# Kernel tuning notes

Hardware: AMD Instinct MI355X
Metric: run time of the kernel (lower is better)

## Reference

```python
import jax, jax.numpy as jnp
import numpy as np

D_MODEL = 1024
D_SAE = 16384
BATCH = 4096
EPS = 1e-8

def _layer_norm(v):
    # v: [B, D]; matches torch branch with keepdim=True
    mean = v.mean(axis=1, keepdims=True)
    var = ((v - mean) ** 2).mean(axis=1, keepdims=True)
    return (v - mean) / jnp.sqrt(var + EPS)

def setup_inputs() -> dict:
    key = jax.random.key(0)
    k1, k2 = jax.random.split(key)
    x = jax.random.normal(k1, (BATCH, 2 * D_MODEL), dtype=jnp.float32)
    # kaiming_uniform on [d_model, d_sae]: bound = sqrt(6 / fan_in), fan_in = d_sae (torch default mode='fan_in' on dim 1)
    bound = float(np.sqrt(6.0 / D_SAE))
    W_enc = jax.random.uniform(k2, (D_MODEL, D_SAE), dtype=jnp.float32, minval=-bound, maxval=bound)
    W_dec = W_enc.T  # init ties decoder to encoder transpose
    b_enc = jnp.zeros((D_SAE,), dtype=jnp.float32)
    b_dec = jnp.zeros((D_MODEL,), dtype=jnp.float32)
    return {"x": x, "W_enc": W_enc, "b_enc": b_enc, "W_dec": W_dec, "b_dec": b_dec, "k": 64}

def reference(x, W_enc, b_enc, W_dec, b_dec, k):
    B = x.shape[0]
    d_model = W_enc.shape[0]
    src = x[:, :d_model]
    tgt = x[:, d_model:]
    # standardize_method == 'layer_norm_and_diff_layer_norm'
    diff = _layer_norm(_layer_norm(tgt) - _layer_norm(src))  # [B, D]
    # encode
    acts = jax.nn.relu(diff @ W_enc + b_enc)  # [B, F]
    # batch top-k on decoder-norm-scaled scores
    dec_norms = jnp.linalg.norm(W_dec, axis=1)  # [F]
    flat_scores = (acts * dec_norms).reshape(-1)  # [B*F]
    _, topk_idx = jax.lax.top_k(flat_scores, k * B)
    mask = jnp.zeros_like(flat_scores).at[topk_idx].set(1.0).reshape(B, -1)
    sparse_acts = acts * mask  # [B, F]
    # decode
    recon = sparse_acts @ W_dec + b_dec  # [B, D]
    return recon
```

## Files before the change

kernel.cpp:

```cpp
#include <hip/hip_runtime.h>
#include <math.h>

#define D_MODEL 1024
#define D_SAE   16384
#define BATCH   4096
#define NTOT    (1ull * BATCH * D_SAE)
#define LN_EPS  1e-8
#define EPS_M   3e-4f
#define ROW_CAP 256
#define CAND_CAP  (4 * 1024 * 1024)
#define CAND2_CAP 65536

using bf16x8 = __attribute__((ext_vector_type(8))) short;
using f32x4  = __attribute__((ext_vector_type(4))) float;

__device__ inline unsigned short f2bf(float f) {
  unsigned u = __float_as_uint(f);
  return (unsigned short)((u + 0x7fffu + ((u >> 16) & 1u)) >> 16);
}
__device__ inline float bf2f(unsigned short h) {
  return __uint_as_float((unsigned)h << 16);
}

__device__ inline double blockReduceSum256(double v, double* lds) {
#pragma unroll
  for (int off = 32; off > 0; off >>= 1) v += __shfl_down(v, off, 64);
  int lane = threadIdx.x & 63, wid = threadIdx.x >> 6;
  __syncthreads();
  if (lane == 0) lds[wid] = v;
  __syncthreads();
  return lds[0] + lds[1] + lds[2] + lds[3];
}
__device__ inline int blockReduceSumInt256(int v, int* lds) {
#pragma unroll
  for (int off = 32; off > 0; off >>= 1) v += __shfl_down(v, off, 64);
  int lane = threadIdx.x & 63, wid = threadIdx.x >> 6;
  __syncthreads();
  if (lane == 0) lds[wid] = v;
  __syncthreads();
  return lds[0] + lds[1] + lds[2] + lds[3];
}

__device__ inline int wave_append(bool pred, int* counter) {
  unsigned long long m = __ballot(pred);
  int lane = threadIdx.x & 63;
  int pos = -1;
  if (m) {
    int ldr = __ffsll((long long)m) - 1;
    int base = 0;
    if (lane == ldr) base = atomicAdd(counter, __popcll(m));
    base = __shfl(base, ldr, 64);
    if (pred) pos = base + __popcll(m & ((1ull << lane) - 1ull));
  }
  return pos;
}

__device__ inline void hist_scan_desc(const int* __restrict__ hist, int nbins, int need,
                                      int& bsel, int& cumsel) {
  int t = threadIdx.x;
  int chunk = nbins >> 6;
  int topbase = nbins - t * chunk;
  int psum = 0;
  for (int i = 1; i <= chunk; ++i) psum += hist[topbase - i];
  int incl = psum;
#pragma unroll
  for (int off = 1; off < 64; off <<= 1) {
    int v = __shfl_up(incl, off, 64);
    if (t >= off) incl += v;
  }
  int excl = incl - psum;
  bool hit = (excl < need) && (excl + psum >= need);
  unsigned long long m = __ballot(hit);
  int tb = m ? (__ffsll((long long)m) - 1) : 63;
  int exb = __shfl(excl, tb, 64);
  int res_b = 0, res_c = 0;
  if (t == tb) {
    int c = exb;
    int b = nbins - tb * chunk - 1;
    int bend = b - chunk;
    for (; b > 0 && b > bend; --b) {
      int cc = hist[b];
      if (c + cc >= need) break;
      c += cc;
    }
    res_b = b; res_c = c;
  }
  bsel = __shfl(res_b, tb, 64);
  cumsel = __shfl(res_c, tb, 64);
}

__device__ inline void ln_row_fp64(const float* __restrict__ row, double* lds, double d[4]) {
  int t = threadIdx.x;
  float4 s4 = *(const float4*)(row + t * 4);
  float4 t4 = *(const float4*)(row + D_MODEL + t * 4);
  double s[4] = {s4.x, s4.y, s4.z, s4.w};
  double tt[4] = {t4.x, t4.y, t4.z, t4.w};
  double ms = blockReduceSum256(s[0] + s[1] + s[2] + s[3], lds) / D_MODEL;
  double mt = blockReduceSum256(tt[0] + tt[1] + tt[2] + tt[3], lds) / D_MODEL;
  double vs = 0, vt = 0;
#pragma unroll
  for (int i = 0; i < 4; i++) { double a = s[i] - ms; vs += a * a; a = tt[i] - mt; vt += a * a; }
  vs = blockReduceSum256(vs, lds) / D_MODEL;
  vt = blockReduceSum256(vt, lds) / D_MODEL;
  double rs = sqrt(vs + LN_EPS), rt = sqrt(vt + LN_EPS);
  double u[4];
#pragma unroll
  for (int i = 0; i < 4; i++) u[i] = (tt[i] - mt) / rt - (s[i] - ms) / rs;
  double mu = blockReduceSum256(u[0] + u[1] + u[2] + u[3], lds) / D_MODEL;
  double vu = 0;
#pragma unroll
  for (int i = 0; i < 4; i++) { double a = u[i] - mu; vu += a * a; }
  vu = blockReduceSum256(vu, lds) / D_MODEL;
  double ru = sqrt(vu + LN_EPS);
#pragma unroll
  for (int i = 0; i < 4; i++) d[i] = (u[i] - mu) / ru;
}

__global__ __launch_bounds__(256) void ln_kernel(const float* __restrict__ x,
                                                 short* __restrict__ Ahi, short* __restrict__ Alo) {
  __shared__ double lds[4];
  int b = blockIdx.x, t = threadIdx.x;
  double d[4];
  ln_row_fp64(x + (size_t)b * (2 * D_MODEL), lds, d);
  int mt = b >> 7, ml = b & 127;
  int ks = t >> 3, kc = (t >> 1) & 3, e0 = (t & 1) * 4;
  size_t base = ((((size_t)mt * 32 + ks) * 4 + kc) * 128 + ml) * 8 + e0;
  short h[4], l[4];
#pragma unroll
  for (int i = 0; i < 4; i++) {
    float f = (float)d[i];
    unsigned short hh = f2bf(f);
    h[i] = (short)hh;
    l[i] = (short)f2bf(f - bf2f(hh));
  }
  *(short4*)&Ahi[base] = make_short4(h[0], h[1], h[2], h[3]);
  *(short4*)&Alo[base] = make_short4(l[0], l[1], l[2], l[3]);
}

__global__ __launch_bounds__(256) void norm_kernel(const float* __restrict__ Wdec,
                                                   double* __restrict__ g64, float* __restrict__ g32) {
  __shared__ double lds[4];
  int j = blockIdx.x, t = threadIdx.x;
  float4 w = *(const float4*)(Wdec + (size_t)j * D_MODEL + t * 4);
  double a = (double)w.x * w.x + (double)w.y * w.y + (double)w.z * w.z + (double)w.w * w.w;
  double sum = blockReduceSum256(a, lds);
  if (t == 0) { double g = sqrt(sum); g64[j] = g; g32[j] = (float)g; }
}

__global__ __launch_bounds__(256) void wsplit_kernel(const float* __restrict__ Wenc,
                                                     short* __restrict__ Whi, short* __restrict__ Wlo) {
  __shared__ short sh[4096];
  __shared__ short sl[4096];
  int blk = blockIdx.x;
  int nt = blk >> 5, ks = blk & 31;
  int t = threadIdx.x;
  int r = t >> 3;
  int cg = t & 7;
  int kc = r >> 3, e = r & 7;
  const float* src = Wenc + (size_t)(ks * 32 + r) * D_SAE + nt * 128 + cg;
#pragma unroll
  for (int j = 0; j < 16; ++j) {
    float f = src[j * 8];
    unsigned short hh = f2bf(f);
    short ll = (short)f2bf(f - bf2f(hh));
    int c = j * 8 + cg;
    sh[kc * 1024 + c * 8 + e] = (short)hh;
    sl[kc * 1024 + c * 8 + e] = ll;
  }
  __syncthreads();
  size_t obase = ((size_t)nt * 32 + ks) * 4096;
  *(float4*)&Whi[obase + t * 16]     = *(const float4*)&sh[t * 16];
  *(float4*)&Whi[obase + t * 16 + 8] = *(const float4*)&sh[t * 16 + 8];
  *(float4*)&Wlo[obase + t * 16]     = *(const float4*)&sl[t * 16];
  *(float4*)&Wlo[obase + t * 16 + 8] = *(const float4*)&sl[t * 16 + 8];
}

__global__ __launch_bounds__(256) void hist_gemm(
    const short* __restrict__ Whi, const short* __restrict__ Ahi,
    const float* __restrict__ benc, const float* __restrict__ g32,
    int* __restrict__ ghist) {
  __shared__ short sA[4096];
  __shared__ short sB[4096];
  __shared__ int h[4][2048];
  const int tid = threadIdx.x;
  const int lane = tid & 63;
  const int w = tid >> 6;
  const int wm = (w >> 1) * 64, wn = (w & 1) * 64;
  int lin = blockIdx.x;
  int mt = lin >> 7, nt = lin & 127;
  const int col0 = nt * 128;
  for (int i = tid; i < 8192; i += 256) ((int*)h)[i] = 0;
  const size_t atile = (size_t)mt * 131072;
  const size_t btile = (size_t)nt * 131072;
  f32x4 acc[4][4] = {};
  const int kcl = lane >> 4, l15 = lane & 15;

  float4 a0, a1, b0, b1;
  {
    const float4* ah4 = (const float4*)(Ahi + atile);
    const float4* bh4 = (const float4*)(Whi + btile);
    a0 = ah4[tid]; a1 = ah4[tid + 256];
    b0 = bh4[tid]; b1 = bh4[tid + 256];
  }
  for (int ks = 0; ks < 32; ++ks) {
    __syncthreads();
    *(float4*)&sA[(size_t)tid * 8] = a0;
    *(float4*)&sA[(size_t)(tid + 256) * 8] = a1;
    *(float4*)&sB[(size_t)tid * 8] = b0;
    *(float4*)&sB[(size_t)(tid + 256) * 8] = b1;
    __syncthreads();
    if (ks < 31) {
      const float4* ah4 = (const float4*)(Ahi + atile + (ks + 1) * 4096);
      const float4* bh4 = (const float4*)(Whi + btile + (ks + 1) * 4096);
      a0 = ah4[tid]; a1 = ah4[tid + 256];
      b0 = bh4[tid]; b1 = bh4[tid + 256];
    }
    bf16x8 ahf[4];
#pragma unroll
    for (int fm = 0; fm < 4; ++fm)
      ahf[fm] = *(const bf16x8*)&sA[(kcl * 128 + wm + fm * 16 + l15) * 8];
#pragma unroll
    for (int fn = 0; fn < 4; ++fn) {
      bf16x8 bh = *(const bf16x8*)&sB[(kcl * 128 + wn + fn * 16 + l15) * 8];
#pragma unroll
      for (int fm = 0; fm < 4; ++fm)
        acc[fm][fn] = __builtin_amdgcn_mfma_f32_16x16x32_bf16(ahf[fm], bh, acc[fm][fn], 0, 0, 0);
    }
  }
#pragma unroll
  for (int fn = 0; fn < 4; ++fn) {
    int col = col0 + wn + fn * 16 + l15;
    float g = g32[col], be = benc[col];
#pragma unroll
    for (int fm = 0; fm < 4; ++fm) {
#pragma unroll
      for (int r = 0; r < 4; ++r) {
        float z = acc[fm][fn][r] + be;
        float s = z > 0.f ? z * g : 0.f;
        unsigned bits = __float_as_uint(s);
        if (bits) atomicAdd(&h[w][bits >> 21], 1);
      }
    }
  }
  __syncthreads();
  for (int i = tid; i < 2048; i += 256) {
    int v = h[0][i] + h[1][i] + h[2][i] + h[3][i];
    if (v) atomicAdd(&ghist[i], v);
  }
}

__global__ __launch_bounds__(512) void mfma_gemm256(
    const short* __restrict__ Whi, const short* __restrict__ Wlo,
    const short* __restrict__ Ahi, const short* __restrict__ Alo,
    const float* __restrict__ benc, const float* __restrict__ g32,
    int* __restrict__ ctrl, int* __restrict__ cand_idx, float* __restrict__ cand_sc,
    int* __restrict__ ghist) {
  __shared__ short sA[16384];
  __shared__ short sB[16384];
  __shared__ int hh[2050];

  const int tid = threadIdx.x;
  const int lane = tid & 63;
  const int w = tid >> 6;
  const int wm = (w >> 2) * 128;
  const int wn = (w & 3) * 64;

  int lin = blockIdx.x;
  int xcd = lin & 7, j = lin >> 3;
  int mt2 = j & 15;
  int nt2 = (xcd << 3) | (j >> 4);
  const int row0 = mt2 * 256, col0 = nt2 * 256;

  const size_t at0 = (size_t)(mt2 * 2) * 131072, at1 = at0 + 131072;
  const size_t bt0 = (size_t)(nt2 * 2) * 131072, bt1 = bt0 + 131072;
  const int dkc = tid >> 7, dml = tid & 127;
  const int dst = (dkc * 256 + dml) * 8;
  const int dst1 = dst + 128 * 8;

  f32x4 acc[8][4] = {};
  const int kcl = lane >> 4, l15 = lane & 15;

  float4 a0, a1, a2, a3, b0, b1, b2, b3;
  {
    a0 = ((const float4*)(Ahi + at0))[tid]; a1 = ((const float4*)(Ahi + at1))[tid];
    a2 = ((const float4*)(Alo + at0))[tid]; a3 = ((const float4*)(Alo + at1))[tid];
    b0 = ((const float4*)(Whi + bt0))[tid]; b1 = ((const float4*)(Whi + bt1))[tid];
    b2 = ((const float4*)(Wlo + bt0))[tid]; b3 = ((const float4*)(Wlo + bt1))[tid];
  }

  for (int ks = 0; ks < 32; ++ks) {
    __syncthreads();
    *(float4*)&sA[dst] = a0;  *(float4*)&sA[dst1] = a1;
    *(float4*)&sA[8192 + dst] = a2;  *(float4*)&sA[8192 + dst1] = a3;
    *(float4*)&sB[dst] = b0;  *(float4*)&sB[dst1] = b1;
    *(float4*)&sB[8192 + dst] = b2;  *(float4*)&sB[8192 + dst1] = b3;
    __syncthreads();
    if (ks < 31) {
      const int o = (ks + 1) * 4096;
      a0 = ((const float4*)(Ahi + at0 + o))[tid]; a1 = ((const float4*)(Ahi + at1 + o))[tid];
      a2 = ((const float4*)(Alo + at0 + o))[tid]; a3 = ((const float4*)(Alo + at1 + o))[tid];
      b0 = ((const float4*)(Whi + bt0 + o))[tid]; b1 = ((const float4*)(Whi + bt1 + o))[tid];
      b2 = ((const float4*)(Wlo + bt0 + o))[tid]; b3 = ((const float4*)(Wlo + bt1 + o))[tid];
    }
    bf16x8 bh[4], bl[4];
#pragma unroll
    for (int fn = 0; fn < 4; ++fn) {
      int boff = (kcl * 256 + wn + fn * 16 + l15) * 8;
      bh[fn] = *(const bf16x8*)&sB[boff];
      bl[fn] = *(const bf16x8*)&sB[8192 + boff];
    }
#pragma unroll
    for (int fm = 0; fm < 8; ++fm) {
      int aoff = (kcl * 256 + wm + fm * 16 + l15) * 8;
      bf16x8 ah = *(const bf16x8*)&sA[aoff];
      bf16x8 al = *(const bf16x8*)&sA[8192 + aoff];
#pragma unroll
      for (int fn = 0; fn < 4; ++fn) {
        acc[fm][fn] = __builtin_amdgcn_mfma_f32_16x16x32_bf16(ah, bh[fn], acc[fm][fn], 0, 0, 0);
        acc[fm][fn] = __builtin_amdgcn_mfma_f32_16x16x32_bf16(al, bh[fn], acc[fm][fn], 0, 0, 0);
        acc[fm][fn] = __builtin_amdgcn_mfma_f32_16x16x32_bf16(ah, bl[fn], acc[fm][fn], 0, 0, 0);
      }
    }
  }

  const int l4r = lane >> 4;
  unsigned thrBits = (unsigned)ctrl[1];
  for (int i = tid; i < 2050; i += 512) hh[i] = 0;
  __syncthreads();
  int cnt = 0;
#pragma unroll
  for (int fn = 0; fn < 4; ++fn) {
    int col = col0 + wn + fn * 16 + l15;
    float g = g32[col], be = benc[col];
#pragma unroll
    for (int fm = 0; fm < 8; ++fm) {
#pragma unroll
      for (int r = 0; r < 4; ++r) {
        float z = acc[fm][fn][r] + be;
        float s = z > 0.f ? z * g : 0.f;
        unsigned bits = __float_as_uint(s);
        if (bits >= thrBits) { cnt++; atomicAdd(&hh[bits >> 21], 1); }
      }
    }
  }
  int my = 0;
  if (cnt) my = atomicAdd(&hh[2048], cnt);
  __syncthreads();
  if (tid == 0) hh[2049] = atomicAdd(&ctrl[2], hh[2048]);
  for (int i = tid; i < 2048; i += 512)
    if (hh[i]) atomicAdd(&ghist[i], hh[i]);
  __syncthreads();
  int pos = hh[2049] + my;
#pragma unroll
  for (int fn = 0; fn < 4; ++fn) {
    int col = col0 + wn + fn * 16 + l15;
    float g = g32[col], be = benc[col];
#pragma unroll
    for (int fm = 0; fm < 8; ++fm) {
      int rowb = row0 + wm + fm * 16 + l4r * 4;
#pragma unroll
      for (int r = 0; r < 4; ++r) {
        float z = acc[fm][fn][r] + be;
        float s = z > 0.f ? z * g : 0.f;
        if (__float_as_uint(s) >= thrBits) {
          if (pos < CAND_CAP) { cand_idx[pos] = (rowb + r) * D_SAE + col; cand_sc[pos] = s; }
          pos++;
        }
      }
    }
  }
}

template <int MODE>
__global__ __launch_bounds__(256) void mfma_gemm(
    const float* __restrict__ Wenc,
    const short* __restrict__ Ahi, const short* __restrict__ Alo,
    const float* __restrict__ benc, const float* __restrict__ g32,
    int* __restrict__ ghist, int* __restrict__ ctrl,
    int* __restrict__ cand_idx, float* __restrict__ cand_sc) {
  __shared__ short sA[8192];
  __shared__ short sB[8192];
  __shared__ int h[(MODE == 0) ? 2048 : 2];
  const int tid = threadIdx.x;
  const int lane = tid & 63;
  const int w = tid >> 6;
  const int wm = (w >> 1) * 64, wn = (w & 1) * 64;
  int lin = blockIdx.x;
  int mt, nt;
  if (MODE == 0) { mt = lin >> 7; nt = lin & 127; }
  else { int xcd = lin & 7, j = lin >> 3; mt = j & 31; nt = (xcd << 4) | (j >> 5); }
  const int row0 = mt * 128, col0 = nt * 128;
  if (MODE == 0) { for (int i = tid; i < 2048; i += 256) h[i] = 0; }
  else if (tid == 0) h[0] = 0;
  const int nl = tid & 127;
  const int half = tid >> 7;
  const float* wbase = Wenc + (size_t)col0 + nl;
  const size_t atile = (size_t)mt * 131072;
  f32x4 acc[4][4] = {};
  const int kcl = lane >> 4, l15 = lane & 15;
  float4 a0, a1, a2, a3;
  float bfv[16];
  {
    const float4* ah4 = (const float4*)(Ahi + atile);
    const float4* al4 = (const float4*)(Alo + atile);
    a0 = ah4[tid]; a1 = ah4[tid + 256];
    a2 = al4[tid]; a3 = al4[tid + 256];
#pragma unroll
    for (int p = 0; p < 4; ++p)
#pragma unroll
      for (int i = 0; i < 4; ++i)
        bfv[p * 4 + i] = wbase[(size_t)(p * 8 + half * 4 + i) * D_SAE];
  }
  for (int ks = 0; ks < 32; ++ks) {
    short hb[16], lb[16];
#pragma unroll
    for (int q = 0; q < 16; ++q) {
      unsigned short hh = f2bf(bfv[q]);
      hb[q] = (short)hh;
      lb[q] = (short)f2bf(bfv[q] - bf2f(hh));
    }
    __syncthreads();
    *(float4*)&sA[(size_t)tid * 8] = a0;
    *(float4*)&sA[(size_t)(tid + 256) * 8] = a1;
    *(float4*)&sA[(size_t)(512 + tid) * 8] = a2;
    *(float4*)&sA[(size_t)(512 + tid + 256) * 8] = a3;
#pragma unroll
    for (int p = 0; p < 4; ++p) {
      int boff = p * 1024 + nl * 8 + half * 4;
      *(short4*)&sB[boff] = make_short4(hb[p * 4], hb[p * 4 + 1], hb[p * 4 + 2], hb[p * 4 + 3]);
      *(short4*)&sB[4096 + boff] = make_short4(lb[p * 4], lb[p * 4 + 1], lb[p * 4 + 2], lb[p * 4 + 3]);
    }
    __syncthreads();
    if (ks < 31) {
      const float4* ah4 = (const float4*)(Ahi + atile + (ks + 1) * 4096);
      const float4* al4 = (const float4*)(Alo + atile + (ks + 1) * 4096);
      a0 = ah4[tid]; a1 = ah4[tid + 256];
      a2 = al4[tid]; a3 = al4[tid + 256];
      const int k0n = (ks + 1) * 32;
#pragma unroll
      for (int p = 0; p < 4; ++p)
#pragma unroll
        for (int i = 0; i < 4; ++i)
          bfv[p * 4 + i] = wbase[(size_t)(k0n + p * 8 + half * 4 + i) * D_SAE];
    }
    bf16x8 ahf[4], alf[4];
#pragma unroll
    for (int fm = 0; fm < 4; ++fm) {
      int off = (kcl * 128 + wm + fm * 16 + l15) * 8;
      ahf[fm] = *(const bf16x8*)&sA[off];
      alf[fm] = *(const bf16x8*)&sA[4096 + off];
    }
#pragma unroll
    for (int fn = 0; fn < 4; ++fn) {
      int boff = (kcl * 128 + wn + fn * 16 + l15) * 8;
      bf16x8 bh = *(const bf16x8*)&sB[boff];
      bf16x8 bl = *(const bf16x8*)&sB[4096 + boff];
#pragma unroll
      for (int fm = 0; fm < 4; ++fm) {
        acc[fm][fn] = __builtin_amdgcn_mfma_f32_16x16x32_bf16(ahf[fm], bh, acc[fm][fn], 0, 0, 0);
        acc[fm][fn] = __builtin_amdgcn_mfma_f32_16x16x32_bf16(alf[fm], bh, acc[fm][fn], 0, 0, 0);
        acc[fm][fn] = __builtin_amdgcn_mfma_f32_16x16x32_bf16(ahf[fm], bl, acc[fm][fn], 0, 0, 0);
      }
    }
  }
  const int l4r = lane >> 4;
  if (MODE == 0) {
#pragma unroll
    for (int fn = 0; fn < 4; ++fn) {
      int col = col0 + wn + fn * 16 + l15;
      float g = g32[col], be = benc[col];
#pragma unroll
      for (int fm = 0; fm < 4; ++fm) {
#pragma unroll
        for (int r = 0; r < 4; ++r) {
          float z = acc[fm][fn][r] + be;
          float s = z > 0.f ? z * g : 0.f;
          unsigned bits = __float_as_uint(s);
          if (bits) atomicAdd(&h[bits >> 21], 1);
        }
      }
    }
    __syncthreads();
    for (int i = tid; i < 2048; i += 256)
      if (h[i]) atomicAdd(&ghist[i], h[i]);
  } else {
    unsigned thrBits = (unsigned)ctrl[1];
    int cnt = 0;
#pragma unroll
    for (int fn = 0; fn < 4; ++fn) {
      int col = col0 + wn + fn * 16 + l15;
      float g = g32[col], be = benc[col];
#pragma unroll
      for (int fm = 0; fm < 4; ++fm) {
#pragma unroll
        for (int r = 0; r < 4; ++r) {
          float z = acc[fm][fn][r] + be;
          float s = z > 0.f ? z * g : 0.f;
          cnt += (__float_as_uint(s) >= thrBits) ? 1 : 0;
        }
      }
    }
    int my = 0;
    if (cnt) my = atomicAdd(&h[0], cnt);
    __syncthreads();
    if (tid == 0) h[1] = atomicAdd(&ctrl[2], h[0]);
    __syncthreads();
    int pos = h[1] + my;
#pragma unroll
    for (int fn = 0; fn < 4; ++fn) {
      int col = col0 + wn + fn * 16 + l15;
      float g = g32[col], be = benc[col];
#pragma unroll
      for (int fm = 0; fm < 4; ++fm) {
        int rowb = row0 + wm + fm * 16 + l4r * 4;
#pragma unroll
        for (int r = 0; r < 4; ++r) {
          float z = acc[fm][fn][r] + be;
          float s = z > 0.f ? z * g : 0.f;
          if (__float_as_uint(s) >= thrBits) {
            if (pos < CAND_CAP) { cand_idx[pos] = (rowb + r) * D_SAE + col; cand_sc[pos] = s; }
            pos++;
          }
        }
      }
    }
  }
}

__global__ void find_coarse_kernel(const int* __restrict__ gh, int* ctrl,
                                   const int* __restrict__ kptr, int sub) {
  long long kB = (long long)kptr[0] * BATCH;
  long long needl = (kB + 500000 + sub - 1) / sub;
  long long fl = 720000 / sub;
  if (needl < fl) needl = fl;
  int b, cum;
  hist_scan_desc(gh, 2048, (int)needl, b, cum);
  if (threadIdx.x == 0) {
    long long est_incl = (long long)sub * (cum + gh[b]);
    if (est_incl > 3500000LL && (long long)sub * cum >= kB + 120000LL) b = b + 1;
    ctrl[1] = (int)(((unsigned)b) << 21);
  }
}

__global__ __launch_bounds__(256) void chist_kernel(const float* __restrict__ cand_sc,
                                                    const int* __restrict__ ctrl,
                                                    int* __restrict__ ghist, int pass) {
  __shared__ int h[2048];
  int nb = (pass == 2) ? 1024 : 2048;
  for (int i = threadIdx.x; i < nb; i += 256) h[i] = 0;
  __syncthreads();
  int n = ctrl[2]; if (n > CAND_CAP) n = CAND_CAP;
  unsigned sel1 = 0, sel22 = 0;
  if (pass == 1) sel1 = (unsigned)ctrl[3];
  if (pass == 2) sel22 = ((unsigned)ctrl[3] << 11) | (unsigned)ctrl[5];
  for (int i = blockIdx.x * 256 + threadIdx.x; i < n; i += gridDim.x * 256) {
    unsigned bits = __float_as_uint(cand_sc[i]);
    if (pass == 0) atomicAdd(&h[bits >> 21], 1);
    else if (pass == 1) { if ((bits >> 21) == sel1) atomicAdd(&h[(bits >> 10) & 0x7FFu], 1); }
    else { if ((bits >> 10) == sel22) atomicAdd(&h[bits & 0x3FFu], 1); }
  }
  __syncthreads();
  for (int i = threadIdx.x; i < nb; i += 256)
    if (h[i]) atomicAdd(&ghist[i], h[i]);
}

__global__ void cfind_kernel(const int* __restrict__ hist, int* ctrl,
                             const int* __restrict__ kptr, int pass) {
  int kB = kptr[0] * BATCH;
  int need, nbins;
  if (pass == 0)      { need = kB;                       nbins = 2048; }
  else if (pass == 1) { need = kB - ctrl[4];             nbins = 2048; }
  else                { need = kB - ctrl[4] - ctrl[6];   nbins = 1024; }
  int b, cum;
  hist_scan_desc(hist, nbins, need, b, cum);
  if (threadIdx.x == 0) {
    if (pass == 0)      { ctrl[3] = b; ctrl[4] = cum; }
    else if (pass == 1) { ctrl[5] = b; ctrl[6] = cum; }
    else {
      unsigned vbits = ((unsigned)ctrl[3] << 21) | ((unsigned)ctrl[5] << 10) | (unsigned)b;
      float V = __uint_as_float(vbits);
      float* cf = (float*)ctrl;
      cf[8] = V; cf[9] = V + EPS_M; cf[10] = V - EPS_M;
    }
  }
}

__global__ __launch_bounds__(256) void band_kernel(const int* __restrict__ cand_idx,
    const float* __restrict__ cand_sc, const float* __restrict__ g32,
    int* ctrl, int* row_cnt, int* row_feat, float* row_act, int* cand2_idx) {
  const float* cf = (const float*)ctrl;
  float hi = cf[9], lo = cf[10];
  int n = ctrl[2]; if (n > CAND_CAP) n = CAND_CAP;
  int lane = threadIdx.x & 63;
  int defc = 0;
  for (int i = blockIdx.x * 256 + threadIdx.x; i < n; i += gridDim.x * 256) {
    float s = cand_sc[i];
    int flat = cand_idx[i];
    if (s > hi) {
      int b = flat >> 14, j = flat & (D_SAE - 1);
      int p = atomicAdd(&row_cnt[b], 1);
      if (p < ROW_CAP) { row_feat[b * ROW_CAP + p] = j; row_act[b * ROW_CAP + p] = s / g32[j]; }
      defc++;
    }
    bool isc = (s <= hi) && (s >= lo);
    int pos = wave_append(isc, &ctrl[12]);
    if (isc && pos >= 0 && pos < CAND2_CAP) cand2_idx[pos] = flat;
  }
#pragma unroll
  for (int off = 32; off > 0; off >>= 1) defc += __shfl_down(defc, off, 64);
  if (lane == 0 && defc) atomicAdd(&ctrl[11], defc);
}

__global__ __launch_bounds__(256) void cand2_score_kernel(const int* __restrict__ ctrl,
    const int* __restrict__ cand2_idx, const float* __restrict__ x,
    const float* __restrict__ Wdec, const float* __restrict__ benc,
    const double* __restrict__ g64, double* __restrict__ cand2_sc) {
  __shared__ double lds[4];
  int n2 = ctrl[12]; if (n2 > CAND2_CAP) n2 = CAND2_CAP;
  int t = threadIdx.x;
  for (int c = blockIdx.x; c < n2; c += gridDim.x) {
    int flat = cand2_idx[c];
    int b = flat >> 14, j = flat & (D_SAE - 1);
    double d[4];
    ln_row_fp64(x + (size_t)b * (2 * D_MODEL), lds, d);
    float4 w4 = *(const float4*)(Wdec + (size_t)j * D_MODEL + t * 4);
    double a = d[0] * (double)w4.x + d[1] * (double)w4.y + d[2] * (double)w4.z + d[3] * (double)w4.w;
    double z = blockReduceSum256(a, lds) + (double)benc[j];
    double sc = z > 0 ? z * g64[j] : 0.0;
    if (t == 0) cand2_sc[c] = sc;
  }
}

__global__ __launch_bounds__(256) void cand2_rank_kernel(const int* __restrict__ ctrl,
    const int* __restrict__ cand2_idx, const double* __restrict__ cand2_sc,
    const double* __restrict__ g64, const int* __restrict__ kptr,
    int* row_cnt, int* row_feat, float* row_act) {
  __shared__ int lds[4];
  int n2 = ctrl[12]; if (n2 > CAND2_CAP) n2 = CAND2_CAP;
  int kB = kptr[0] * BATCH;
  int fill = kB - ctrl[11];
  int t = threadIdx.x;
  for (int c = blockIdx.x; c < n2; c += gridDim.x) {
    double sc = cand2_sc[c];
    int fc = cand2_idx[c];
    int cnt = 0;
    for (int y = t; y < n2; y += 256) {
      double sy = cand2_sc[y];
      if (sy > sc || (sy == sc && cand2_idx[y] < fc)) cnt++;
    }
    cnt = blockReduceSumInt256(cnt, lds);
    if (t == 0 && cnt < fill) {
      int b = fc >> 14, j = fc & (D_SAE - 1);
      int p = atomicAdd(&row_cnt[b], 1);
      if (p < ROW_CAP) { row_feat[b * ROW_CAP + p] = j; row_act[b * ROW_CAP + p] = (float)(sc / g64[j]); }
    }
  }
}

__global__ __launch_bounds__(256) void recon_kernel(const int* __restrict__ row_cnt,
    const int* __restrict__ row_feat, const float* __restrict__ row_act,
    const float* __restrict__ Wdec, const float* __restrict__ bdec, float* __restrict__ out) {
  int b = blockIdx.x, t = threadIdx.x;
  float4 acc0 = *(const float4*)&bdec[t * 4];
  float4 acc1 = make_float4(0.f, 0.f, 0.f, 0.f);
  int n = row_cnt[b]; if (n > ROW_CAP) n = ROW_CAP;
  const int* rf = row_feat + (size_t)b * ROW_CAP;
  const float* ra = row_act + (size_t)b * ROW_CAP;
  int p = 0;
  for (; p + 2 <= n; p += 2) {
    int j0 = rf[p], j1 = rf[p + 1];
    float v0 = ra[p], v1 = ra[p + 1];
    float4 w0 = *(const float4*)(Wdec + (size_t)j0 * D_MODEL + t * 4);
    float4 w1 = *(const float4*)(Wdec + (size_t)j1 * D_MODEL + t * 4);
    acc0.x += v0 * w0.x; acc0.y += v0 * w0.y; acc0.z += v0 * w0.z; acc0.w += v0 * w0.w;
    acc1.x += v1 * w1.x; acc1.y += v1 * w1.y; acc1.z += v1 * w1.z; acc1.w += v1 * w1.w;
  }
  if (p < n) {
    int j0 = rf[p]; float v0 = ra[p];
    float4 w0 = *(const float4*)(Wdec + (size_t)j0 * D_MODEL + t * 4);
    acc0.x += v0 * w0.x; acc0.y += v0 * w0.y; acc0.z += v0 * w0.z; acc0.w += v0 * w0.w;
  }
  acc0.x += acc1.x; acc0.y += acc1.y; acc0.z += acc1.z; acc0.w += acc1.w;
  *(float4*)(out + (size_t)b * D_MODEL + t * 4) = acc0;
}

extern "C" void kernel_launch(void* const* d_in, const int* in_sizes, int n_in,
                              void* d_out, int out_size, void* d_ws, size_t ws_size,
                              hipStream_t stream) {
  const float* x    = (const float*)d_in[0];
  const float* Wenc = (const float*)d_in[1];
  const float* benc = (const float*)d_in[2];
  const float* Wdec = (const float*)d_in[3];
  const float* bdec = (const float*)d_in[4];
  const int*   kptr = (const int*)d_in[5];
  float* out = (float*)d_out;

  char* ws = (char*)d_ws;
  size_t off = 0;
  short*  Ahi       = (short*)(ws + off);  off += (size_t)BATCH * D_MODEL * 2;
  short*  Alo       = (short*)(ws + off);  off += (size_t)BATCH * D_MODEL * 2;
  int*    cand_idx  = (int*)(ws + off);    off += (size_t)CAND_CAP * 4;
  float*  cand_sc   = (float*)(ws + off);  off += (size_t)CAND_CAP * 4;
  int*    row_feat  = (int*)(ws + off);    off += (size_t)BATCH * ROW_CAP * 4;
  float*  row_act   = (float*)(ws + off);  off += (size_t)BATCH * ROW_CAP * 4;
  int*    cand2_idx = (int*)(ws + off);    off += (size_t)CAND2_CAP * 4;
  double* cand2_sc  = (double*)(ws + off); off += (size_t)CAND2_CAP * 8;
  double* g64       = (double*)(ws + off); off += (size_t)D_SAE * 8;
  float*  g32       = (float*)(ws + off);  off += (size_t)D_SAE * 4;
  char*   zbase     = ws + off;
  int* ghist   = (int*)(zbase);
  int* h1      = (int*)(zbase + 8192);
  int* h2      = (int*)(zbase + 16384);
  int* h3      = (int*)(zbase + 24576);
  int* ctrl    = (int*)(zbase + 28672);
  int* row_cnt = (int*)(zbase + 28928);
  size_t zbytes = 28928 + (size_t)BATCH * 4;
  size_t small_need = off + zbytes;
  if (small_need > ws_size) return;

  size_t big_off = (small_need + 255) & ~(size_t)255;
  short* Whi = (short*)(ws + big_off);
  short* Wlo = Whi + (size_t)D_MODEL * D_SAE;
  size_t big_need = big_off + (size_t)D_MODEL * D_SAE * 4;
  const bool big = (big_need <= ws_size);

  hipMemsetAsync(zbase, 0, zbytes, stream);

  ln_kernel<<<BATCH, 256, 0, stream>>>(x, Ahi, Alo);
  norm_kernel<<<D_SAE, 256, 0, stream>>>(Wdec, g64, g32);
  if (big) {
    wsplit_kernel<<<4096, 256, 0, stream>>>(Wenc, Whi, Wlo);
    hist_gemm<<<512, 256, 0, stream>>>(Whi, Ahi, benc, g32, ghist);
    find_coarse_kernel<<<1, 64, 0, stream>>>(ghist, ctrl, kptr, 8);
    mfma_gemm256<<<1024, 512, 0, stream>>>(Whi, Wlo, Ahi, Alo, benc, g32, ctrl, cand_idx, cand_sc, h1);
  } else {
    mfma_gemm<0><<<256, 256, 0, stream>>>(Wenc, Ahi, Alo, benc, g32, ghist, ctrl, nullptr, nullptr);
    find_coarse_kernel<<<1, 64, 0, stream>>>(ghist, ctrl, kptr, 16);
    mfma_gemm<1><<<4096, 256, 0, stream>>>(Wenc, Ahi, Alo, benc, g32, nullptr, ctrl, cand_idx, cand_sc);
    chist_kernel<<<1024, 256, 0, stream>>>(cand_sc, ctrl, h1, 0);
  }
  cfind_kernel<<<1, 64, 0, stream>>>(h1, ctrl, kptr, 0);
  chist_kernel<<<1024, 256, 0, stream>>>(cand_sc, ctrl, h2, 1);
  cfind_kernel<<<1, 64, 0, stream>>>(h2, ctrl, kptr, 1);
  chist_kernel<<<1024, 256, 0, stream>>>(cand_sc, ctrl, h3, 2);
  cfind_kernel<<<1, 64, 0, stream>>>(h3, ctrl, kptr, 2);
  band_kernel<<<1024, 256, 0, stream>>>(cand_idx, cand_sc, g32, ctrl, row_cnt, row_feat, row_act, cand2_idx);
  cand2_score_kernel<<<4096, 256, 0, stream>>>(ctrl, cand2_idx, x, Wdec, benc, g64, cand2_sc);
  cand2_rank_kernel<<<2048, 256, 0, stream>>>(ctrl, cand2_idx, cand2_sc, g64, kptr, row_cnt, row_feat, row_act);
  recon_kernel<<<BATCH, 256, 0, stream>>>(row_cnt, row_feat, row_act, Wdec, bdec, out);
}
```

Before: 754.4 us.

## Double-buffer GEMM tiles via direct global-to-LDS loads; one wave per row in norm

The main split-bf16 GEMM now stages tiles with global_load_lds (direct global-to-LDS DMA) into two LDS buffers, prefetching the next k-step while the current one feeds the MFMAs. This replaces the register round-trip and one of the two barriers per iteration. The cost is doubled LDS (128 KB for A and B), which may reduce occupancy. Separately, the decoder-norm kernel computes one row per wavefront with shuffle reductions, launching four times fewer blocks and avoiding LDS and block-level syncs.

```diff
diff --git a/kernel.cpp b/kernel.cpp
--- a/kernel.cpp
+++ b/kernel.cpp
@@ -20,6 +20,12 @@
 }
 __device__ inline float bf2f(unsigned short h) {
   return __uint_as_float((unsigned)h << 16);
+}
+
+__device__ inline void gll16(const short* g, char* l) {
+  __builtin_amdgcn_global_load_lds(
+      (const __attribute__((address_space(1))) void*)g,
+      (__attribute__((address_space(3))) void*)l, 16, 0, 0);
 }
 
 __device__ inline double blockReduceSum256(double v, double* lds) {
@@ -139,12 +145,18 @@
 
 __global__ __launch_bounds__(256) void norm_kernel(const float* __restrict__ Wdec,
                                                    double* __restrict__ g64, float* __restrict__ g32) {
-  __shared__ double lds[4];
-  int j = blockIdx.x, t = threadIdx.x;
-  float4 w = *(const float4*)(Wdec + (size_t)j * D_MODEL + t * 4);
-  double a = (double)w.x * w.x + (double)w.y * w.y + (double)w.z * w.z + (double)w.w * w.w;
-  double sum = blockReduceSum256(a, lds);
-  if (t == 0) { double g = sqrt(sum); g64[j] = g; g32[j] = (float)g; }
+  int wv = threadIdx.x >> 6, lane = threadIdx.x & 63;
+  int j = (blockIdx.x << 2) | wv;
+  const float4* rowp = (const float4*)(Wdec + (size_t)j * D_MODEL);
+  double a = 0;
+#pragma unroll
+  for (int q = 0; q < 4; ++q) {
+    float4 w = rowp[lane + q * 64];
+    a += (double)w.x * w.x + (double)w.y * w.y + (double)w.z * w.z + (double)w.w * w.w;
+  }
+#pragma unroll
+  for (int off = 32; off > 0; off >>= 1) a += __shfl_down(a, off, 64);
+  if (lane == 0) { double g = sqrt(a); g64[j] = g; g32[j] = (float)g; }
 }
 
 __global__ __launch_bounds__(256) void wsplit_kernel(const float* __restrict__ Wenc,
@@ -255,8 +267,8 @@
     const float* __restrict__ benc, const float* __restrict__ g32,
     int* __restrict__ ctrl, int* __restrict__ cand_idx, float* __restrict__ cand_sc,
     int* __restrict__ ghist) {
-  __shared__ short sA[16384];
-  __shared__ short sB[16384];
+  __shared__ short sAraw[32768];
+  __shared__ short sBraw[32768];
   __shared__ int hh[2050];
 
   const int tid = threadIdx.x;
@@ -273,47 +285,54 @@
 
   const size_t at0 = (size_t)(mt2 * 2) * 131072, at1 = at0 + 131072;
   const size_t bt0 = (size_t)(nt2 * 2) * 131072, bt1 = bt0 + 131072;
-  const int dkc = tid >> 7, dml = tid & 127;
-  const int dst = (dkc * 256 + dml) * 8;
-  const int dst1 = dst + 128 * 8;
+
+  const short* gAh0 = Ahi + at0 + (size_t)tid * 8;
+  const short* gAh1 = Ahi + at1 + (size_t)tid * 8;
+  const short* gAl0 = Alo + at0 + (size_t)tid * 8;
+  const short* gAl1 = Alo + at1 + (size_t)tid * 8;
+  const short* gBh0 = Whi + bt0 + (size_t)tid * 8;
+  const short* gBh1 = Whi + bt1 + (size_t)tid * 8;
+  const short* gBl0 = Wlo + bt0 + (size_t)tid * 8;
+  const short* gBl1 = Wlo + bt1 + (size_t)tid * 8;
+  const int dstB = (tid >> 7) * 4096 + (tid & 127) * 16;
+
+  auto stage = [&](int bsel, int ksn) {
+    const size_t o = (size_t)ksn * 4096;
+    char* ab = (char*)sAraw + bsel * 32768 + dstB;
+    char* bb = (char*)sBraw + bsel * 32768 + dstB;
+    gll16(gAh0 + o, ab);
+    gll16(gAh1 + o, ab + 2048);
+    gll16(gAl0 + o, ab + 16384);
+    gll16(gAl1 + o, ab + 16384 + 2048);
+    gll16(gBh0 + o, bb);
+    gll16(gBh1 + o, bb + 2048);
+    gll16(gBl0 + o, bb + 16384);
+    gll16(gBl1 + o, bb + 16384 + 2048);
+  };
 
   f32x4 acc[8][4] = {};
   const int kcl = lane >> 4, l15 = lane & 15;
 
-  float4 a0, a1, a2, a3, b0, b1, b2, b3;
-  {
-    a0 = ((const float4*)(Ahi + at0))[tid]; a1 = ((const float4*)(Ahi + at1))[tid];
-    a2 = ((const float4*)(Alo + at0))[tid]; a3 = ((const float4*)(Alo + at1))[tid];
-    b0 = ((const float4*)(Whi + bt0))[tid]; b1 = ((const float4*)(Whi + bt1))[tid];
-    b2 = ((const float4*)(Wlo + bt0))[tid]; b3 = ((const float4*)(Wlo + bt1))[tid];
-  }
+  stage(0, 0);
+  __syncthreads();
+  int cur = 0;
 
   for (int ks = 0; ks < 32; ++ks) {
-    __syncthreads();
-    *(float4*)&sA[dst] = a0;  *(float4*)&sA[dst1] = a1;
-    *(float4*)&sA[8192 + dst] = a2;  *(float4*)&sA[8192 + dst1] = a3;
-    *(float4*)&sB[dst] = b0;  *(float4*)&sB[dst1] = b1;
-    *(float4*)&sB[8192 + dst] = b2;  *(float4*)&sB[8192 + dst1] = b3;
-    __syncthreads();
-    if (ks < 31) {
-      const int o = (ks + 1) * 4096;
-      a0 = ((const float4*)(Ahi + at0 + o))[tid]; a1 = ((const float4*)(Ahi + at1 + o))[tid];
-      a2 = ((const float4*)(Alo + at0 + o))[tid]; a3 = ((const float4*)(Alo + at1 + o))[tid];
-      b0 = ((const float4*)(Whi + bt0 + o))[tid]; b1 = ((const float4*)(Whi + bt1 + o))[tid];
-      b2 = ((const float4*)(Wlo + bt0 + o))[tid]; b3 = ((const float4*)(Wlo + bt1 + o))[tid];
-    }
+    if (ks < 31) stage(cur ^ 1, ks + 1);
+    const short* tA = sAraw + cur * 16384;
+    const short* tB = sBraw + cur * 16384;
     bf16x8 bh[4], bl[4];
 #pragma unroll
     for (int fn = 0; fn < 4; ++fn) {
       int boff = (kcl * 256 + wn + fn * 16 + l15) * 8;
-      bh[fn] = *(const bf16x8*)&sB[boff];
-      bl[fn] = *(const bf16x8*)&sB[8192 + boff];
+      bh[fn] = *(const bf16x8*)&tB[boff];
+      bl[fn] = *(const bf16x8*)&tB[8192 + boff];
     }
 #pragma unroll
     for (int fm = 0; fm < 8; ++fm) {
       int aoff = (kcl * 256 + wm + fm * 16 + l15) * 8;
-      bf16x8 ah = *(const bf16x8*)&sA[aoff];
-      bf16x8 al = *(const bf16x8*)&sA[8192 + aoff];
+      bf16x8 ah = *(const bf16x8*)&tA[aoff];
+      bf16x8 al = *(const bf16x8*)&tA[8192 + aoff];
 #pragma unroll
       for (int fn = 0; fn < 4; ++fn) {
         acc[fm][fn] = __builtin_amdgcn_mfma_f32_16x16x32_bf16(ah, bh[fn], acc[fm][fn], 0, 0, 0);
@@ -321,6 +340,8 @@
         acc[fm][fn] = __builtin_amdgcn_mfma_f32_16x16x32_bf16(ah, bl[fn], acc[fm][fn], 0, 0, 0);
       }
     }
+    __syncthreads();
+    cur ^= 1;
   }
 
   const int l4r = lane >> 4;
@@ -727,7 +748,7 @@
   hipMemsetAsync(zbase, 0, zbytes, stream);
 
   ln_kernel<<<BATCH, 256, 0, stream>>>(x, Ahi, Alo);
-  norm_kernel<<<D_SAE, 256, 0, stream>>>(Wdec, g64, g32);
+  norm_kernel<<<D_SAE / 4, 256, 0, stream>>>(Wdec, g64, g32);
   if (big) {
     wsplit_kernel<<<4096, 256, 0, stream>>>(Wenc, Whi, Wlo);
     hist_gemm<<<512, 256, 0, stream>>>(Whi, Ahi, benc, g32, ghist);
```

Result: no change. 762.4 us (+1.1%).

## Shrink extraction GEMM tile to 128x128 and use wave-per-row decoder norm

Applied to the files above, without the earlier changes.

The main split-bf16 GEMM that extracts top-k candidates moves from 256x256 tiles with 512 threads to 128x128 tiles with 256 threads. It launches four times as many blocks, uses half the LDS, and holds fewer accumulators, which should raise occupancy and let waves hide latency better. The cost is lower arithmetic intensity, so each block reloads more operand data from global memory. Separately, the decoder-norm kernel now computes one row per wavefront with shuffle reductions instead of one row per block, cutting block count and LDS synchronization.

```diff
diff --git a/kernel.cpp b/kernel.cpp
--- a/kernel.cpp
+++ b/kernel.cpp
@@ -139,12 +139,18 @@
 
 __global__ __launch_bounds__(256) void norm_kernel(const float* __restrict__ Wdec,
                                                    double* __restrict__ g64, float* __restrict__ g32) {
-  __shared__ double lds[4];
-  int j = blockIdx.x, t = threadIdx.x;
-  float4 w = *(const float4*)(Wdec + (size_t)j * D_MODEL + t * 4);
-  double a = (double)w.x * w.x + (double)w.y * w.y + (double)w.z * w.z + (double)w.w * w.w;
-  double sum = blockReduceSum256(a, lds);
-  if (t == 0) { double g = sqrt(sum); g64[j] = g; g32[j] = (float)g; }
+  int wv = threadIdx.x >> 6, lane = threadIdx.x & 63;
+  int j = (blockIdx.x << 2) | wv;
+  const float4* rowp = (const float4*)(Wdec + (size_t)j * D_MODEL);
+  double a = 0;
+#pragma unroll
+  for (int q = 0; q < 4; ++q) {
+    float4 w = rowp[lane + q * 64];
+    a += (double)w.x * w.x + (double)w.y * w.y + (double)w.z * w.z + (double)w.w * w.w;
+  }
+#pragma unroll
+  for (int off = 32; off > 0; off >>= 1) a += __shfl_down(a, off, 64);
+  if (lane == 0) { double g = sqrt(a); g64[j] = g; g32[j] = (float)g; }
 }
 
 __global__ __launch_bounds__(256) void wsplit_kernel(const float* __restrict__ Wenc,
@@ -249,83 +255,92 @@
   }
 }
 
-__global__ __launch_bounds__(512) void mfma_gemm256(
+__global__ __launch_bounds__(256) void extract_gemm128(
     const short* __restrict__ Whi, const short* __restrict__ Wlo,
     const short* __restrict__ Ahi, const short* __restrict__ Alo,
     const float* __restrict__ benc, const float* __restrict__ g32,
     int* __restrict__ ctrl, int* __restrict__ cand_idx, float* __restrict__ cand_sc,
     int* __restrict__ ghist) {
-  __shared__ short sA[16384];
-  __shared__ short sB[16384];
+  __shared__ short sA[8192];
+  __shared__ short sB[8192];
   __shared__ int hh[2050];
 
   const int tid = threadIdx.x;
   const int lane = tid & 63;
   const int w = tid >> 6;
-  const int wm = (w >> 2) * 128;
-  const int wn = (w & 3) * 64;
+  const int wm = (w >> 1) * 64, wn = (w & 1) * 64;
 
   int lin = blockIdx.x;
   int xcd = lin & 7, j = lin >> 3;
-  int mt2 = j & 15;
-  int nt2 = (xcd << 3) | (j >> 4);
-  const int row0 = mt2 * 256, col0 = nt2 * 256;
-
-  const size_t at0 = (size_t)(mt2 * 2) * 131072, at1 = at0 + 131072;
-  const size_t bt0 = (size_t)(nt2 * 2) * 131072, bt1 = bt0 + 131072;
-  const int dkc = tid >> 7, dml = tid & 127;
-  const int dst = (dkc * 256 + dml) * 8;
-  const int dst1 = dst + 128 * 8;
-
-  f32x4 acc[8][4] = {};
+  int mt = j & 31;
+  int nt = (xcd << 4) | (j >> 5);
+  const int row0 = mt * 128, col0 = nt * 128;
+
+  const size_t atile = (size_t)mt * 131072;
+  const size_t btile = (size_t)nt * 131072;
+
+  f32x4 acc[4][4] = {};
   const int kcl = lane >> 4, l15 = lane & 15;
 
   float4 a0, a1, a2, a3, b0, b1, b2, b3;
   {
-    a0 = ((const float4*)(Ahi + at0))[tid]; a1 = ((const float4*)(Ahi + at1))[tid];
-    a2 = ((const float4*)(Alo + at0))[tid]; a3 = ((const float4*)(Alo + at1))[tid];
-    b0 = ((const float4*)(Whi + bt0))[tid]; b1 = ((const float4*)(Whi + bt1))[tid];
-    b2 = ((const float4*)(Wlo + bt0))[tid]; b3 = ((const float4*)(Wlo + bt1))[tid];
+    const float4* ah4 = (const float4*)(Ahi + atile);
+    const float4* al4 = (const float4*)(Alo + atile);
+    const float4* bh4 = (const float4*)(Whi + btile);
+    const float4* bl4 = (const float4*)(Wlo + btile);
+    a0 = ah4[tid]; a1 = ah4[tid + 256];
+    a2 = al4[tid]; a3 = al4[tid + 256];
+    b0 = bh4[tid]; b1 = bh4[tid + 256];
+    b2 = bl4[tid]; b3 = bl4[tid + 256];
   }
 
   for (int ks = 0; ks < 32; ++ks) {
     __syncthreads();
-    *(float4*)&sA[dst] = a0;  *(float4*)&sA[dst1] = a1;
-    *(float4*)&sA[8192 + dst] = a2;  *(float4*)&sA[8192 + dst1] = a3;
-    *(float4*)&sB[dst] = b0;  *(float4*)&sB[dst1] = b1;
-    *(float4*)&sB[8192 + dst] = b2;  *(float4*)&sB[8192 + dst1] = b3;
+    *(float4*)&sA[(size_t)tid * 8] = a0;
+    *(float4*)&sA[(size_t)(tid + 256) * 8] = a1;
+    *(float4*)&sA[(size_t)(512 + tid) * 8] = a2;
+    *(float4*)&sA[(size_t)(512 + tid + 256) * 8] = a3;
+    *(float4*)&sB[(size_t)tid * 8] = b0;
+    *(float4*)&sB[(size_t)(tid + 256) * 8] = b1;
+    *(float4*)&sB[(size_t)(512 + tid) * 8] = b2;
+    *(float4*)&sB[(size_t)(512 + tid + 256) * 8] = b3;
     __syncthreads();
     if (ks < 31) {
       const int o = (ks + 1) * 4096;
-      a0 = ((const float4*)(Ahi + at0 + o))[tid]; a1 = ((const float4*)(Ahi + at1 + o))[tid];
-      a2 = ((const float4*)(Alo + at0 + o))[tid]; a3 = ((const float4*)(Alo + at1 + o))[tid];
-      b0 = ((const float4*)(Whi + bt0 + o))[tid]; b1 = ((const float4*)(Whi + bt1 + o))[tid];
-      b2 = ((const float4*)(Wlo + bt0 + o))[tid]; b3 = ((const float4*)(Wlo + bt1 + o))[tid];
-    }
-    bf16x8 bh[4], bl[4];
+      const float4* ah4 = (const float4*)(Ahi + atile + o);
+      const float4* al4 = (const float4*)(Alo + atile + o);
+      const float4* bh4 = (const float4*)(Whi + btile + o);
+      const float4* bl4 = (const float4*)(Wlo + btile + o);
+      a0 = ah4[tid]; a1 = ah4[tid + 256];
+      a2 = al4[tid]; a3 = al4[tid + 256];
+      b0 = bh4[tid]; b1 = bh4[tid + 256];
+      b2 = bl4[tid]; b3 = bl4[tid + 256];
+    }
+    bf16x8 ahf[4], alf[4];
+#pragma unroll
+    for (int fm = 0; fm < 4; ++fm) {
+      int off = (kcl * 128 + wm + fm * 16 + l15) * 8;
+      ahf[fm] = *(const bf16x8*)&sA[off];
+      alf[fm] = *(const bf16x8*)&sA[4096 + off];
+    }
 #pragma unroll
     for (int fn = 0; fn < 4; ++fn) {
-      int boff = (kcl * 256 + wn + fn * 16 + l15) * 8;
-      bh[fn] = *(const bf16x8*)&sB[boff];
-      bl[fn] = *(const bf16x8*)&sB[8192 + boff];
-    }
-#pragma unroll
-    for (int fm = 0; fm < 8; ++fm) {
-      int aoff = (kcl * 256 + wm + fm * 16 + l15) * 8;
-      bf16x8 ah = *(const bf16x8*)&sA[aoff];
-      bf16x8 al = *(const bf16x8*)&sA[8192 + aoff];
-#pragma unroll
-      for (int fn = 0; fn < 4; ++fn) {
-        acc[fm][fn] = __builtin_amdgcn_mfma_f32_16x16x32_bf16(ah, bh[fn], acc[fm][fn], 0, 0, 0);
-        acc[fm][fn] = __builtin_amdgcn_mfma_f32_16x16x32_bf16(al, bh[fn], acc[fm][fn], 0, 0, 0);
-        acc[fm][fn] = __builtin_amdgcn_mfma_f32_16x16x32_bf16(ah, bl[fn], acc[fm][fn], 0, 0, 0);
+      int boff = (kcl * 128 + wn + fn * 16 + l15) * 8;
+      bf16x8 bh = *(const bf16x8*)&sB[boff];
+      bf16x8 bl = *(const bf16x8*)&sB[4096 + boff];
+#pragma unroll
+      for (int fm = 0; fm < 4; ++fm) {
+        acc[fm][fn] = __builtin_amdgcn_mfma_f32_16x16x32_bf16(ahf[fm], bh, acc[fm][fn], 0, 0, 0);
+        acc[fm][fn] = __builtin_amdgcn_mfma_f32_16x16x32_bf16(alf[fm], bh, acc[fm][fn], 0, 0, 0);
+        acc[fm][fn] = __builtin_amdgcn_mfma_f32_16x16x32_bf16(ahf[fm], bl, acc[fm][fn], 0, 0, 0);
       }
     }
   }
 
   const int l4r = lane >> 4;
   unsigned thrBits = (unsigned)ctrl[1];
-  for (int i = tid; i < 2050; i += 512) hh[i] = 0;
+  __syncthreads();
+  for (int i = tid; i < 2050; i += 256) hh[i] = 0;
   __syncthreads();
   int cnt = 0;
 #pragma unroll
@@ -333,7 +348,7 @@
     int col = col0 + wn + fn * 16 + l15;
     float g = g32[col], be = benc[col];
 #pragma unroll
-    for (int fm = 0; fm < 8; ++fm) {
+    for (int fm = 0; fm < 4; ++fm) {
 #pragma unroll
       for (int r = 0; r < 4; ++r) {
         float z = acc[fm][fn][r] + be;
@@ -347,7 +362,7 @@
   if (cnt) my = atomicAdd(&hh[2048], cnt);
   __syncthreads();
   if (tid == 0) hh[2049] = atomicAdd(&ctrl[2], hh[2048]);
-  for (int i = tid; i < 2048; i += 512)
+  for (int i = tid; i < 2048; i += 256)
     if (hh[i]) atomicAdd(&ghist[i], hh[i]);
   __syncthreads();
   int pos = hh[2049] + my;
@@ -356,7 +371,7 @@
     int col = col0 + wn + fn * 16 + l15;
     float g = g32[col], be = benc[col];
 #pragma unroll
-    for (int fm = 0; fm < 8; ++fm) {
+    for (int fm = 0; fm < 4; ++fm) {
       int rowb = row0 + wm + fm * 16 + l4r * 4;
 #pragma unroll
       for (int r = 0; r < 4; ++r) {
@@ -727,12 +742,12 @@
   hipMemsetAsync(zbase, 0, zbytes, stream);
 
   ln_kernel<<<BATCH, 256, 0, stream>>>(x, Ahi, Alo);
-  norm_kernel<<<D_SAE, 256, 0, stream>>>(Wdec, g64, g32);
+  norm_kernel<<<D_SAE / 4, 256, 0, stream>>>(Wdec, g64, g32);
   if (big) {
     wsplit_kernel<<<4096, 256, 0, stream>>>(Wenc, Whi, Wlo);
     hist_gemm<<<512, 256, 0, stream>>>(Whi, Ahi, benc, g32, ghist);
     find_coarse_kernel<<<1, 64, 0, stream>>>(ghist, ctrl, kptr, 8);
-    mfma_gemm256<<<1024, 512, 0, stream>>>(Whi, Wlo, Ahi, Alo, benc, g32, ctrl, cand_idx, cand_sc, h1);
+    extract_gemm128<<<4096, 256, 0, stream>>>(Whi, Wlo, Ahi, Alo, benc, g32, ctrl, cand_idx, cand_sc, h1);
   } else {
     mfma_gemm<0><<<256, 256, 0, stream>>>(Wenc, Ahi, Alo, benc, g32, ghist, ctrl, nullptr, nullptr);
     find_coarse_kernel<<<1, 64, 0, stream>>>(ghist, ctrl, kptr, 16);
```

Result: slower. 844.2 us (+11.9%).
